# Optimization experiments

Measured on AMD Instinct MI355X. Metric: run time of the kernel, lower is better.

Reference implementation:

```python
import jax, jax.numpy as jnp
import numpy as np

K = 3      # kernel size (fixed by 18 = 2*K*K offset channels)
PAD = 1
EPS = 1e-5 # BatchNorm eps


def setup_inputs() -> dict:
    key = jax.random.key(0)
    ks = jax.random.split(key, 4)
    B, Cin, Cout, H, W = 8, 64, 64, 96, 96
    x = jax.random.normal(ks[0], (B, Cin, H, W), jnp.float32)
    # small offset-conv weights so predicted offsets stay within a few pixels
    w_off = jax.random.normal(ks[1], (2 * K * K, Cin, K, K), jnp.float32) * 0.02
    b_off = jnp.zeros((2 * K * K,), jnp.float32)
    w_def = jax.random.normal(ks[2], (Cout, Cin, K, K), jnp.float32) * (1.0 / np.sqrt(Cin * K * K))
    b_def = jnp.zeros((Cout,), jnp.float32)
    gamma = jnp.ones((Cout,), jnp.float32)
    beta = jnp.zeros((Cout,), jnp.float32)
    return dict(x=x, w_off=w_off, b_off=b_off, w_def=w_def, b_def=b_def, gamma=gamma, beta=beta)


def _deform_sample(x, offset):
    """Bilinear-sample x at deformed kernel tap locations.
    x: (B,C,H,W); offset: (B,2*K*K,H,W) with (dy,dx) pairs per tap, row-major.
    Returns (B,C,K*K,H,W). Out-of-bounds samples are zero (torchvision semantics).
    """
    B, C, H, W = x.shape
    off = offset.reshape(B, K * K, 2, H, W)
    dy, dx = off[:, :, 0], off[:, :, 1]              # (B,9,H,W)
    ky = (jnp.arange(K * K) // K).astype(x.dtype)    # tap row index
    kx = (jnp.arange(K * K) % K).astype(x.dtype)     # tap col index
    base_y = jnp.arange(H, dtype=x.dtype)[:, None] - PAD   # (H,1)
    base_x = jnp.arange(W, dtype=x.dtype)[None, :] - PAD   # (1,W)
    py = dy + ky[None, :, None, None] + base_y[None, None]  # (B,9,H,W)
    px = dx + kx[None, :, None, None] + base_x[None, None]
    y0 = jnp.floor(py)
    x0 = jnp.floor(px)
    wy1 = py - y0
    wx1 = px - x0
    wy0 = 1.0 - wy1
    wx0 = 1.0 - wx1
    xflat = x.reshape(B, C, H * W)
    acc = jnp.zeros((B, C, K * K * H * W), x.dtype)
    corners = [(y0, x0, wy0 * wx0), (y0, x0 + 1.0, wy0 * wx1),
               (y0 + 1.0, x0, wy1 * wx0), (y0 + 1.0, x0 + 1.0, wy1 * wx1)]
    for yc, xc, wc in corners:
        valid = (yc >= 0) & (yc <= H - 1) & (xc >= 0) & (xc <= W - 1)
        iy = jnp.clip(yc, 0, H - 1).astype(jnp.int32)
        ix = jnp.clip(xc, 0, W - 1).astype(jnp.int32)
        idx = (iy * W + ix).reshape(B, 1, K * K * H * W)
        v = jnp.take_along_axis(xflat, idx, axis=2)          # (B,C,9HW) gather
        w = jnp.where(valid, wc, 0.0).reshape(B, 1, K * K * H * W)
        acc = acc + v * w
    return acc.reshape(B, C, K * K, H, W)


def reference(x, w_off, b_off, w_def, b_def, gamma, beta):
    # 1) offset-predicting conv
    offset = jax.lax.conv_general_dilated(
        x, w_off, window_strides=(1, 1), padding=((PAD, PAD), (PAD, PAD)),
        dimension_numbers=("NCHW", "OIHW", "NCHW")) + b_off[None, :, None, None]
    # 2) deformable conv: bilinear gather then per-pixel contraction over (C, taps)
    sampled = _deform_sample(x, offset)                      # (B,C,9,H,W)
    Cout = w_def.shape[0]
    y = jnp.einsum("bckhw,ock->bohw", sampled, w_def.reshape(Cout, -1, K * K))
    y = y + b_def[None, :, None, None]
    # 3) BatchNorm2d (training mode: batch statistics) + ReLU
    mean = y.mean(axis=(0, 2, 3))
    var = y.var(axis=(0, 2, 3))
    y = (y - mean[None, :, None, None]) * jax.lax.rsqrt(var[None, :, None, None] + EPS)
    y = gamma[None, :, None, None] * y + beta[None, :, None, None]
    return jax.nn.relu(y)
```

## Files before the change

### kernel.cpp

```cpp
#include <hip/hip_runtime.h>
#include <hip/hip_bf16.h>
#include <stdint.h>

static constexpr int NBATCH = 8;
static constexpr int Cin  = 64;
static constexpr int Cout = 64;
static constexpr int H = 96, W = 96;
static constexpr int HW   = H * W;
static constexpr int NPIX = NBATCH * HW;
static constexpr int NBLK = NPIX / 64;
static constexpr int BLK_PER_BATCH = HW / 64;
static constexpr float EPS = 1e-5f;

typedef short    bf16x8 __attribute__((ext_vector_type(8)));
typedef float    f32x4  __attribute__((ext_vector_type(4)));
typedef uint32_t u32x4  __attribute__((ext_vector_type(4)));

__device__ inline uint16_t f2bf(float f) {
    __hip_bfloat16 h = __float2bfloat16(f);
    return *reinterpret_cast<uint16_t*>(&h);
}
__device__ inline float bf2f(uint16_t u) {
    union { uint32_t i; float f; } z;
    z.i = ((uint32_t)u) << 16;
    return z.f;
}
__device__ inline float lo_bf(uint32_t w) {
    union { uint32_t i; float f; } z; z.i = w << 16; return z.f;
}
__device__ inline float hi_bf(uint32_t w) {
    union { uint32_t i; float f; } z; z.i = w & 0xffff0000u; return z.f;
}
__device__ inline uint32_t pack_trunc(float lo, float hi) {
    union { float f; uint32_t i; } a, b;
    a.f = lo; b.f = hi;
    return (b.i & 0xffff0000u) | (a.i >> 16);
}
__device__ inline void gld_lds16(const void* g, void* l) {
    __builtin_amdgcn_global_load_lds(
        (const __attribute__((address_space(1))) void*)g,
        (__attribute__((address_space(3))) void*)l, 16, 0, 0);
}

__global__ __launch_bounds__(256) void transpose_pack(
        const float* __restrict__ x,
        const float* __restrict__ w_off,
        const float* __restrict__ w_def,
        uint16_t* __restrict__ xT,
        uint16_t* __restrict__ woffPack,
        uint16_t* __restrict__ wdefPack,
        float* __restrict__ zeropage) {
    int t = blockIdx.x * 256 + threadIdx.x;
    int pix  = t >> 1;
    int half = t & 1;
    int b = pix / HW, rem = pix % HW;
    const float* xb = x + (size_t)(b * Cin) * HW + rem + (size_t)(half * 32) * HW;
    uint16_t* o = xT + (size_t)pix * 64 + half * 32;
#pragma unroll
    for (int cg = 0; cg < 4; ++cg) {
        bf16x8 v;
#pragma unroll
        for (int e = 0; e < 8; ++e) v[e] = (short)f2bf(xb[(cg * 8 + e) * HW]);
        *reinterpret_cast<bf16x8*>(o + cg * 8) = v;
    }
    if (blockIdx.x < 64) {
        int t0 = blockIdx.x * 256 + threadIdx.x;
        if (t0 < 64) zeropage[t0] = 0.f;
        for (int i = t0; i < 72 * 32 * 8; i += 64 * 256) {
            int e = i & 7;
            int n = (i >> 3) & 31;
            int sg = i >> 8;
            int k = sg * 8 + e;
            int tap = k >> 6, c = k & 63;
            woffPack[i] = (n < 18) ? f2bf(w_off[(n * Cin + c) * 9 + tap]) : (uint16_t)0;
        }
        for (int i = t0; i < 72 * 64 * 8; i += 64 * 256) {
            int e = i & 7;
            int n = (i >> 3) & 63;
            int sg = i >> 9;
            int k = sg * 8 + e;
            int tap = k >> 6, c = k & 63;
            wdefPack[i] = f2bf(w_def[(n * Cin + c) * 9 + tap]);
        }
    }
}

#define P3_SETUP(T, W00,W01,W10,W11,I00,I01,I10,I11)                        \
    if ((T) < 8) {                                                          \
        int src_ = lanebase + (T);                                          \
        W00 = __shfl(w00a, src_); W01 = __shfl(w01a, src_);                 \
        W10 = __shfl(w10a, src_); W11 = __shfl(w11a, src_);                 \
        I00 = __shfl(i00a, src_); I01 = __shfl(i01a, src_);                 \
        I10 = __shfl(i10a, src_); I11 = __shfl(i11a, src_);                 \
    } else {                                                                \
        W00 = w00b; W01 = w01b; W10 = w10b; W11 = w11b;                     \
        I00 = i00b; I01 = i01b; I10 = i10b; I11 = i11b;                     \
    }

#define P3_ISSUE(I00,I01,I10,I11,C00,C01,C10,C11)                           \
    C00 = *reinterpret_cast<const u32x4*>(basep + (I00) * 64);              \
    C01 = *reinterpret_cast<const u32x4*>(basep + (I01) * 64);              \
    C10 = *reinterpret_cast<const u32x4*>(basep + (I10) * 64);              \
    C11 = *reinterpret_cast<const u32x4*>(basep + (I11) * 64);

#define P3_CONV(T, W00,W01,W10,W11,C00,C01,C10,C11)                         \
    {                                                                       \
        u32x4 outv_;                                                        \
        _Pragma("unroll")                                                   \
        for (int i = 0; i < 4; ++i) {                                       \
            float slo_ = (W00) * lo_bf((C00)[i]) + (W01) * lo_bf((C01)[i])  \
                       + (W10) * lo_bf((C10)[i]) + (W11) * lo_bf((C11)[i]); \
            float shi_ = (W00) * hi_bf((C00)[i]) + (W01) * hi_bf((C01)[i])  \
                       + (W10) * hi_bf((C10)[i]) + (W11) * hi_bf((C11)[i]); \
            outv_[i] = pack_trunc(slo_, shi_);                              \
        }                                                                   \
        *reinterpret_cast<u32x4*>(&As[(((T) * 64 + pr) * 8 + slot) * 8]) = outv_; \
    }

__global__ __launch_bounds__(512, 4) void fused_deform(
        const uint16_t* __restrict__ xT,
        const uint16_t* __restrict__ woffPack,
        const uint16_t* __restrict__ wdefPack,
        const float* __restrict__ b_off,
        const float* __restrict__ zeropage,
        uint16_t* __restrict__ ybf,
        float* __restrict__ partial) {
    __shared__ __attribute__((aligned(16))) char smem[73728];
    __shared__ float offs[64 * 18];
    __shared__ float s_red[128];
    short* As   = (short*)smem;
    float* osum = (float*)smem;
    float* red  = (float*)smem;

    int tid  = threadIdx.x;
    int lane = tid & 63;
    int wv   = tid >> 6;
    int l15  = lane & 15;
    int lg   = lane >> 4;

    int wgid  = (blockIdx.x & 7) * BLK_PER_BATCH + (blockIdx.x >> 3);
    int gpix0 = wgid * 64;
    int b     = gpix0 / HW;
    int rem0  = gpix0 % HW;
    const uint16_t* xTb = xT + (size_t)b * HW * 64;

    int pr   = (wv << 3) + (lane >> 3);
    int e8   = lane & 7;
    int slot = e8 ^ (pr & 7);
    int remP = rem0 + pr;
    int hP   = remP / W, wP = remP % W;

    {
        const uint16_t* gsrc = xTb + slot * 8;
        char* ldsbase = (char*)As + (size_t)wv * 1024;
#pragma unroll
        for (int tap = 0; tap < 9; ++tap) {
            int yy = hP + tap / 3 - 1;
            int xx = wP + tap % 3 - 1;
            bool ok = (yy >= 0) && (yy < H) && (xx >= 0) && (xx < W);
            const void* g = ok ? (const void*)(gsrc + (yy * W + xx) * 64)
                               : (const void*)zeropage;
            gld_lds16(g, ldsbase + tap * 8192);
        }
    }
    __syncthreads();

    {
        int wj = wv & 1;
        int kq = wv >> 1;
        int sbeg = (kq < 2) ? kq * 5 : 2 + kq * 4;
        int send = (kq < 2) ? sbeg + 5 : sbeg + 4;
        f32x4 oacc[4];
#pragma unroll
        for (int m = 0; m < 4; ++m) oacc[m] = (f32x4){0.f, 0.f, 0.f, 0.f};
        __builtin_amdgcn_s_setprio(1);
        for (int s = sbeg; s < send; ++s) {
            int sg = s * 4 + lg;
            bf16x8 bb = *reinterpret_cast<const bf16x8*>(
                woffPack + (sg * 32 + wj * 16 + l15) * 8);
#pragma unroll
            for (int m = 0; m < 4; ++m) {
                bf16x8 a = *reinterpret_cast<const bf16x8*>(
                    &As[(((sg >> 3) * 64 + m * 16 + l15) * 8 + ((sg & 7) ^ (l15 & 7))) * 8]);
                oacc[m] = __builtin_amdgcn_mfma_f32_16x16x32_bf16(a, bb, oacc[m], 0, 0, 0);
            }
        }
        __builtin_amdgcn_s_setprio(0);
        __syncthreads();
#pragma unroll
        for (int m = 0; m < 4; ++m)
#pragma unroll
            for (int r = 0; r < 4; ++r)
                osum[(kq * 64 + m * 16 + lg * 4 + r) * 34 + wj * 16 + l15] = oacc[m][r];
        __syncthreads();
        for (int i = tid; i < 64 * 18; i += 512) {
            int rr = i / 18, o = i - rr * 18;
            offs[i] = osum[rr * 34 + o] + osum[(64 + rr) * 34 + o]
                    + osum[(128 + rr) * 34 + o] + osum[(192 + rr) * 34 + o] + b_off[o];
        }
        if (tid < 128) s_red[tid] = 0.f;
        __syncthreads();
    }

    {
        float hm1 = (float)(hP - 1), wm1 = (float)(wP - 1);
        float w00a, w01a, w10a, w11a; int i00a, i01a, i10a, i11a;
        {
            int t = e8;
            int ty = (t * 11) >> 5;
            int tx = t - 3 * ty;
            float dy = offs[pr * 18 + 2 * t];
            float dx = offs[pr * 18 + 2 * t + 1];
            float py = dy + (float)ty + hm1;
            float px = dx + (float)tx + wm1;
            float y0f = floorf(py), x0f = floorf(px);
            float wy1 = py - y0f, wx1 = px - x0f;
            float wy0 = 1.f - wy1, wx0 = 1.f - wx1;
            int iy0 = (int)y0f, ix0 = (int)x0f;
            int iy1 = iy0 + 1,  ix1 = ix0 + 1;
            bool vy0 = (iy0 >= 0) && (iy0 < H), vy1 = (iy1 >= 0) && (iy1 < H);
            bool vx0 = (ix0 >= 0) && (ix0 < W), vx1 = (ix1 >= 0) && (ix1 < W);
            w00a = (vy0 && vx0) ? wy0 * wx0 : 0.f;
            w01a = (vy0 && vx1) ? wy0 * wx1 : 0.f;
            w10a = (vy1 && vx0) ? wy1 * wx0 : 0.f;
            w11a = (vy1 && vx1) ? wy1 * wx1 : 0.f;
            int cy0 = min(max(iy0, 0), H - 1), cy1 = min(max(iy1, 0), H - 1);
            int cx0 = min(max(ix0, 0), W - 1), cx1 = min(max(ix1, 0), W - 1);
            i00a = cy0 * W + cx0; i01a = cy0 * W + cx1;
            i10a = cy1 * W + cx0; i11a = cy1 * W + cx1;
        }
        float w00b, w01b, w10b, w11b; int i00b, i01b, i10b, i11b;
        {
            float dy = offs[pr * 18 + 16];
            float dx = offs[pr * 18 + 17];
            float py = dy + 2.f + hm1;
            float px = dx + 2.f + wm1;
            float y0f = floorf(py), x0f = floorf(px);
            float wy1 = py - y0f, wx1 = px - x0f;
            float wy0 = 1.f - wy1, wx0 = 1.f - wx1;
            int iy0 = (int)y0f, ix0 = (int)x0f;
            int iy1 = iy0 + 1,  ix1 = ix0 + 1;
            bool vy0 = (iy0 >= 0) && (iy0 < H), vy1 = (iy1 >= 0) && (iy1 < H);
            bool vx0 = (ix0 >= 0) && (ix0 < W), vx1 = (ix1 >= 0) && (ix1 < W);
            w00b = (vy0 && vx0) ? wy0 * wx0 : 0.f;
            w01b = (vy0 && vx1) ? wy0 * wx1 : 0.f;
            w10b = (vy1 && vx0) ? wy1 * wx0 : 0.f;
            w11b = (vy1 && vx1) ? wy1 * wx1 : 0.f;
            int cy0 = min(max(iy0, 0), H - 1), cy1 = min(max(iy1, 0), H - 1);
            int cx0 = min(max(ix0, 0), W - 1), cx1 = min(max(ix1, 0), W - 1);
            i00b = cy0 * W + cx0; i01b = cy0 * W + cx1;
            i10b = cy1 * W + cx0; i11b = cy1 * W + cx1;
        }

        const uint16_t* basep = xTb + e8 * 8;
        int lanebase = lane & 56;

        float uA0,uA1,uA2,uA3; int jA0,jA1,jA2,jA3; u32x4 cA0,cA1,cA2,cA3;
        float uB0,uB1,uB2,uB3; int jB0,jB1,jB2,jB3; u32x4 cB0,cB1,cB2,cB3;

        P3_SETUP(0, uA0,uA1,uA2,uA3, jA0,jA1,jA2,jA3)
        P3_ISSUE(jA0,jA1,jA2,jA3, cA0,cA1,cA2,cA3)
        P3_SETUP(1, uB0,uB1,uB2,uB3, jB0,jB1,jB2,jB3)
        P3_ISSUE(jB0,jB1,jB2,jB3, cB0,cB1,cB2,cB3)
        P3_CONV(0, uA0,uA1,uA2,uA3, cA0,cA1,cA2,cA3)
        P3_SETUP(2, uA0,uA1,uA2,uA3, jA0,jA1,jA2,jA3)
        P3_ISSUE(jA0,jA1,jA2,jA3, cA0,cA1,cA2,cA3)
        P3_CONV(1, uB0,uB1,uB2,uB3, cB0,cB1,cB2,cB3)
        P3_SETUP(3, uB0,uB1,uB2,uB3, jB0,jB1,jB2,jB3)
        P3_ISSUE(jB0,jB1,jB2,jB3, cB0,cB1,cB2,cB3)
        P3_CONV(2, uA0,uA1,uA2,uA3, cA0,cA1,cA2,cA3)
        P3_SETUP(4, uA0,uA1,uA2,uA3, jA0,jA1,jA2,jA3)
        P3_ISSUE(jA0,jA1,jA2,jA3, cA0,cA1,cA2,cA3)
        P3_CONV(3, uB0,uB1,uB2,uB3, cB0,cB1,cB2,cB3)
        P3_SETUP(5, uB0,uB1,uB2,uB3, jB0,jB1,jB2,jB3)
        P3_ISSUE(jB0,jB1,jB2,jB3, cB0,cB1,cB2,cB3)
        P3_CONV(4, uA0,uA1,uA2,uA3, cA0,cA1,cA2,cA3)
        P3_SETUP(6, uA0,uA1,uA2,uA3, jA0,jA1,jA2,jA3)
        P3_ISSUE(jA0,jA1,jA2,jA3, cA0,cA1,cA2,cA3)
        P3_CONV(5, uB0,uB1,uB2,uB3, cB0,cB1,cB2,cB3)
        P3_SETUP(7, uB0,uB1,uB2,uB3, jB0,jB1,jB2,jB3)
        P3_ISSUE(jB0,jB1,jB2,jB3, cB0,cB1,cB2,cB3)
        P3_CONV(6, uA0,uA1,uA2,uA3, cA0,cA1,cA2,cA3)
        P3_SETUP(8, uA0,uA1,uA2,uA3, jA0,jA1,jA2,jA3)
        P3_ISSUE(jA0,jA1,jA2,jA3, cA0,cA1,cA2,cA3)
        P3_CONV(7, uB0,uB1,uB2,uB3, cB0,cB1,cB2,cB3)
        P3_CONV(8, uA0,uA1,uA2,uA3, cA0,cA1,cA2,cA3)
    }
    __syncthreads();

    {
        int nf = wv & 3;
        int kh = wv >> 2;
        f32x4 acc[4];
#pragma unroll
        for (int m = 0; m < 4; ++m) acc[m] = (f32x4){0.f, 0.f, 0.f, 0.f};
        __builtin_amdgcn_s_setprio(1);
#pragma unroll
        for (int s = 0; s < 9; ++s) {
            int sg = (kh * 9 + s) * 4 + lg;
            bf16x8 bb = *reinterpret_cast<const bf16x8*>(
                wdefPack + (sg * 64 + nf * 16 + l15) * 8);
#pragma unroll
            for (int m = 0; m < 4; ++m) {
                bf16x8 a = *reinterpret_cast<const bf16x8*>(
                    &As[(((sg >> 3) * 64 + m * 16 + l15) * 8 + ((sg & 7) ^ (l15 & 7))) * 8]);
                acc[m] = __builtin_amdgcn_mfma_f32_16x16x32_bf16(a, bb, acc[m], 0, 0, 0);
            }
        }
        __builtin_amdgcn_s_setprio(0);
        __syncthreads();
#pragma unroll
        for (int m = 0; m < 4; ++m)
#pragma unroll
            for (int r = 0; r < 4; ++r)
                red[(kh * 64 + m * 16 + lg * 4 + r) * 66 + nf * 16 + l15] = acc[m][r];
        __syncthreads();

        int c  = lane;
        int rg = wv;
        bf16x8 ov;
        float s = 0.f, q = 0.f;
#pragma unroll
        for (int k2 = 0; k2 < 8; ++k2) {
            int r = rg * 8 + k2;
            float v = red[r * 66 + c] + red[(64 + r) * 66 + c];
            ov[k2] = (short)f2bf(v);
            s += v; q += v * v;
        }
        *reinterpret_cast<bf16x8*>(
            ybf + ((size_t)b * Cout + c) * HW + rem0 + rg * 8) = ov;
        atomicAdd(&s_red[c], s);
        atomicAdd(&s_red[64 + c], q);
    }
    __syncthreads();
    if (tid < 128) partial[(size_t)wgid * 128 + tid] = s_red[tid];
}

__global__ __launch_bounds__(256) void bn_reduce1(const float* __restrict__ partial,
                                                  float* __restrict__ partial2) {
    __shared__ float red[256];
    int ch = threadIdx.x & 127;
    int g  = threadIdx.x >> 7;
    float s = 0.f;
#pragma unroll
    for (int r = 0; r < 8; ++r)
        s += partial[(size_t)(blockIdx.x * 16 + g * 8 + r) * 128 + ch];
    red[threadIdx.x] = s;
    __syncthreads();
    if (g == 0)
        partial2[(size_t)blockIdx.x * 128 + ch] = red[ch] + red[128 + ch];
}

__global__ void bn_stats2(const float* __restrict__ partial2,
                          const float* __restrict__ gamma,
                          const float* __restrict__ beta,
                          float* __restrict__ stats) {
    __shared__ float red[256];
    int ch = threadIdx.x & 127;
    int g  = threadIdx.x >> 7;
    float s = 0.f;
    for (int i = 0; i < 36; ++i)
        s += partial2[(size_t)(g * 36 + i) * 128 + ch];
    red[threadIdx.x] = s;
    __syncthreads();
    if (threadIdx.x < 64) {
        int c = threadIdx.x;
        float sum = red[c] + red[128 + c];
        float sq  = red[64 + c] + red[192 + c];
        float mean = sum / (float)NPIX;
        float var  = sq / (float)NPIX - mean * mean;
        float v    = var + EPS;
        float inv  = rsqrtf(v);
        inv = inv * (1.5f - 0.5f * v * inv * inv);
        float sc = gamma[c] * inv;
        stats[c]      = sc;
        stats[64 + c] = beta[c] - mean * sc;
    }
}

__global__ __launch_bounds__(256) void bn_apply(const uint16_t* __restrict__ ybf,
                                                float* __restrict__ out,
                                                const float* __restrict__ stats) {
    int t = blockIdx.x * blockDim.x + threadIdx.x;
    int e = t * 8;
    int ch = (e / HW) & 63;
    float sc = stats[ch];
    float sh = stats[64 + ch];
    bf16x8 v = *reinterpret_cast<const bf16x8*>(ybf + e);
    f32x4 o0, o1;
#pragma unroll
    for (int i = 0; i < 4; ++i) {
        o0[i] = fmaxf(bf2f((uint16_t)v[i])     * sc + sh, 0.f);
        o1[i] = fmaxf(bf2f((uint16_t)v[4 + i]) * sc + sh, 0.f);
    }
    *reinterpret_cast<f32x4*>(out + e)     = o0;
    *reinterpret_cast<f32x4*>(out + e + 4) = o1;
}

extern "C" void kernel_launch(void* const* d_in, const int* in_sizes, int n_in,
                              void* d_out, int out_size, void* d_ws, size_t ws_size,
                              hipStream_t stream) {
    const float* x     = (const float*)d_in[0];
    const float* w_off = (const float*)d_in[1];
    const float* b_off = (const float*)d_in[2];
    const float* w_def = (const float*)d_in[3];
    const float* gamma = (const float*)d_in[5];
    const float* beta  = (const float*)d_in[6];
    float* out = (float*)d_out;
    char*  ws  = (char*)d_ws;

    uint16_t* xT       = (uint16_t*)ws;
    uint16_t* woffPack = (uint16_t*)(ws + 9437184);
    uint16_t* wdefPack = (uint16_t*)(ws + 9474048);
    float*    partial  = (float*)(ws + 9547776);
    float*    partial2 = (float*)(ws + 10137600);
    float*    stats    = (float*)(ws + 10174464);
    float*    zeropage = (float*)(ws + 10174976);
    uint16_t* ybf      = (uint16_t*)(ws + 10175232);

    transpose_pack<<<NPIX * 2 / 256, 256, 0, stream>>>(x, w_off, w_def, xT,
                                                       woffPack, wdefPack, zeropage);
    fused_deform<<<NBLK, 512, 0, stream>>>(xT, woffPack, wdefPack, b_off,
                                           zeropage, ybf, partial);
    bn_reduce1<<<72, 256, 0, stream>>>(partial, partial2);
    bn_stats2<<<1, 256, 0, stream>>>(partial2, gamma, beta, stats);
    bn_apply<<<(NPIX * Cout / 8) / 256, 256, 0, stream>>>(ybf, out, stats);
}
```

Before: 61.44 us.

## Shrink fused deform tile to 48 pixels with 384-thread blocks and re-split MFMA work

Changes the per-block pixel tile from 64 to 48, using 6 waves (384 threads) instead of 8, and re-partitions both MFMA phases so each wave handles a K-third and two output-column fragments (3x2 accumulators) rather than one. The grid grows to 1536 blocks, which is meant to improve load balance across CUs and reduce LDS per block. The BN reduction launch sizes and workspace offsets are adjusted to match. The trade-off is fewer blocks per CU by launch bounds (3 instead of 4), a three-way K reduction through LDS, and more B-fragment reuse per wave but also more register pressure.

```diff
diff --git a/kernel.cpp b/kernel.cpp
--- a/kernel.cpp
+++ b/kernel.cpp
@@ -8,8 +8,9 @@
 static constexpr int H = 96, W = 96;
 static constexpr int HW   = H * W;
 static constexpr int NPIX = NBATCH * HW;
-static constexpr int NBLK = NPIX / 64;
-static constexpr int BLK_PER_BATCH = HW / 64;
+static constexpr int NTILE = 48;
+static constexpr int NBLK = NPIX / NTILE;
+static constexpr int BLK_PER_BATCH = HW / NTILE;
 static constexpr float EPS = 1e-5f;
 
 typedef short    bf16x8 __attribute__((ext_vector_type(8)));
@@ -114,10 +115,10 @@
                        + (W10) * hi_bf((C10)[i]) + (W11) * hi_bf((C11)[i]); \
             outv_[i] = pack_trunc(slo_, shi_);                              \
         }                                                                   \
-        *reinterpret_cast<u32x4*>(&As[(((T) * 64 + pr) * 8 + slot) * 8]) = outv_; \
-    }
-
-__global__ __launch_bounds__(512, 4) void fused_deform(
+        *reinterpret_cast<u32x4*>(&As[(((T) * NTILE + pr) * 8 + slot) * 8]) = outv_; \
+    }
+
+__global__ __launch_bounds__(384, 3) void fused_deform(
         const uint16_t* __restrict__ xT,
         const uint16_t* __restrict__ woffPack,
         const uint16_t* __restrict__ wdefPack,
@@ -125,8 +126,8 @@
         const float* __restrict__ zeropage,
         uint16_t* __restrict__ ybf,
         float* __restrict__ partial) {
-    __shared__ __attribute__((aligned(16))) char smem[73728];
-    __shared__ float offs[64 * 18];
+    __shared__ __attribute__((aligned(16))) char smem[72 * NTILE * 16];
+    __shared__ float offs[NTILE * 18];
     __shared__ float s_red[128];
     short* As   = (short*)smem;
     float* osum = (float*)smem;
@@ -139,13 +140,12 @@
     int lg   = lane >> 4;
 
     int wgid  = (blockIdx.x & 7) * BLK_PER_BATCH + (blockIdx.x >> 3);
-    int gpix0 = wgid * 64;
-    int b     = gpix0 / HW;
-    int rem0  = gpix0 % HW;
+    int b     = blockIdx.x & 7;
+    int rem0  = (wgid - b * BLK_PER_BATCH) * NTILE;
     const uint16_t* xTb = xT + (size_t)b * HW * 64;
 
-    int pr   = (wv << 3) + (lane >> 3);
-    int e8   = lane & 7;
+    int pr   = tid >> 3;
+    int e8   = tid & 7;
     int slot = e8 ^ (pr & 7);
     int remP = rem0 + pr;
     int hP   = remP / W, wP = remP % W;
@@ -160,43 +160,41 @@
             bool ok = (yy >= 0) && (yy < H) && (xx >= 0) && (xx < W);
             const void* g = ok ? (const void*)(gsrc + (yy * W + xx) * 64)
                                : (const void*)zeropage;
-            gld_lds16(g, ldsbase + tap * 8192);
+            gld_lds16(g, ldsbase + tap * (NTILE * 128));
         }
     }
     __syncthreads();
 
     {
         int wj = wv & 1;
-        int kq = wv >> 1;
-        int sbeg = (kq < 2) ? kq * 5 : 2 + kq * 4;
-        int send = (kq < 2) ? sbeg + 5 : sbeg + 4;
-        f32x4 oacc[4];
-#pragma unroll
-        for (int m = 0; m < 4; ++m) oacc[m] = (f32x4){0.f, 0.f, 0.f, 0.f};
+        int kt = wv >> 1;
+        f32x4 oacc[3];
+#pragma unroll
+        for (int m = 0; m < 3; ++m) oacc[m] = (f32x4){0.f, 0.f, 0.f, 0.f};
         __builtin_amdgcn_s_setprio(1);
-        for (int s = sbeg; s < send; ++s) {
+        for (int s = kt * 6; s < kt * 6 + 6; ++s) {
             int sg = s * 4 + lg;
             bf16x8 bb = *reinterpret_cast<const bf16x8*>(
                 woffPack + (sg * 32 + wj * 16 + l15) * 8);
 #pragma unroll
-            for (int m = 0; m < 4; ++m) {
+            for (int m = 0; m < 3; ++m) {
                 bf16x8 a = *reinterpret_cast<const bf16x8*>(
-                    &As[(((sg >> 3) * 64 + m * 16 + l15) * 8 + ((sg & 7) ^ (l15 & 7))) * 8]);
+                    &As[(((sg >> 3) * NTILE + m * 16 + l15) * 8 + ((sg & 7) ^ (l15 & 7))) * 8]);
                 oacc[m] = __builtin_amdgcn_mfma_f32_16x16x32_bf16(a, bb, oacc[m], 0, 0, 0);
             }
         }
         __builtin_amdgcn_s_setprio(0);
         __syncthreads();
 #pragma unroll
-        for (int m = 0; m < 4; ++m)
+        for (int m = 0; m < 3; ++m)
 #pragma unroll
             for (int r = 0; r < 4; ++r)
-                osum[(kq * 64 + m * 16 + lg * 4 + r) * 34 + wj * 16 + l15] = oacc[m][r];
+                osum[(kt * NTILE + m * 16 + lg * 4 + r) * 34 + wj * 16 + l15] = oacc[m][r];
         __syncthreads();
-        for (int i = tid; i < 64 * 18; i += 512) {
+        for (int i = tid; i < NTILE * 18; i += 384) {
             int rr = i / 18, o = i - rr * 18;
-            offs[i] = osum[rr * 34 + o] + osum[(64 + rr) * 34 + o]
-                    + osum[(128 + rr) * 34 + o] + osum[(192 + rr) * 34 + o] + b_off[o];
+            offs[i] = osum[rr * 34 + o] + osum[(NTILE + rr) * 34 + o]
+                    + osum[(2 * NTILE + rr) * 34 + o] + b_off[o];
         }
         if (tid < 128) s_red[tid] = 0.f;
         __syncthreads();
@@ -289,41 +287,51 @@
     __syncthreads();
 
     {
-        int nf = wv & 3;
-        int kh = wv >> 2;
-        f32x4 acc[4];
-#pragma unroll
-        for (int m = 0; m < 4; ++m) acc[m] = (f32x4){0.f, 0.f, 0.f, 0.f};
+        int npair = wv & 1;
+        int kt = wv >> 1;
+        f32x4 acc[3][2];
+#pragma unroll
+        for (int m = 0; m < 3; ++m)
+#pragma unroll
+            for (int jj = 0; jj < 2; ++jj) acc[m][jj] = (f32x4){0.f, 0.f, 0.f, 0.f};
         __builtin_amdgcn_s_setprio(1);
 #pragma unroll
-        for (int s = 0; s < 9; ++s) {
-            int sg = (kh * 9 + s) * 4 + lg;
-            bf16x8 bb = *reinterpret_cast<const bf16x8*>(
-                wdefPack + (sg * 64 + nf * 16 + l15) * 8);
-#pragma unroll
-            for (int m = 0; m < 4; ++m) {
-                bf16x8 a = *reinterpret_cast<const bf16x8*>(
-                    &As[(((sg >> 3) * 64 + m * 16 + l15) * 8 + ((sg & 7) ^ (l15 & 7))) * 8]);
-                acc[m] = __builtin_amdgcn_mfma_f32_16x16x32_bf16(a, bb, acc[m], 0, 0, 0);
+        for (int s0 = 0; s0 < 6; ++s0) {
+            int sg = (kt * 6 + s0) * 4 + lg;
+#pragma unroll
+            for (int jj = 0; jj < 2; ++jj) {
+                int nf = npair * 2 + jj;
+                bf16x8 bb = *reinterpret_cast<const bf16x8*>(
+                    wdefPack + (sg * 64 + nf * 16 + l15) * 8);
+#pragma unroll
+                for (int m = 0; m < 3; ++m) {
+                    bf16x8 a = *reinterpret_cast<const bf16x8*>(
+                        &As[(((sg >> 3) * NTILE + m * 16 + l15) * 8 + ((sg & 7) ^ (l15 & 7))) * 8]);
+                    acc[m][jj] = __builtin_amdgcn_mfma_f32_16x16x32_bf16(a, bb, acc[m][jj], 0, 0, 0);
+                }
             }
         }
         __builtin_amdgcn_s_setprio(0);
         __syncthreads();
 #pragma unroll
-        for (int m = 0; m < 4; ++m)
-#pragma unroll
-            for (int r = 0; r < 4; ++r)
-                red[(kh * 64 + m * 16 + lg * 4 + r) * 66 + nf * 16 + l15] = acc[m][r];
+        for (int m = 0; m < 3; ++m)
+#pragma unroll
+            for (int jj = 0; jj < 2; ++jj)
+#pragma unroll
+                for (int r = 0; r < 4; ++r)
+                    red[(kt * NTILE + m * 16 + lg * 4 + r) * 66
+                        + (npair * 2 + jj) * 16 + l15] = acc[m][jj][r];
         __syncthreads();
 
-        int c  = lane;
-        int rg = wv;
+        int c  = tid & 63;
+        int rg = tid >> 6;
         bf16x8 ov;
         float s = 0.f, q = 0.f;
 #pragma unroll
         for (int k2 = 0; k2 < 8; ++k2) {
             int r = rg * 8 + k2;
-            float v = red[r * 66 + c] + red[(64 + r) * 66 + c];
+            float v = red[r * 66 + c] + red[(NTILE + r) * 66 + c]
+                    + red[(2 * NTILE + r) * 66 + c];
             ov[k2] = (short)f2bf(v);
             s += v; q += v * v;
         }
@@ -359,8 +367,8 @@
     int ch = threadIdx.x & 127;
     int g  = threadIdx.x >> 7;
     float s = 0.f;
-    for (int i = 0; i < 36; ++i)
-        s += partial2[(size_t)(g * 36 + i) * 128 + ch];
+    for (int i = 0; i < 48; ++i)
+        s += partial2[(size_t)(g * 48 + i) * 128 + ch];
     red[threadIdx.x] = s;
     __syncthreads();
     if (threadIdx.x < 64) {
@@ -413,16 +421,16 @@
     uint16_t* woffPack = (uint16_t*)(ws + 9437184);
     uint16_t* wdefPack = (uint16_t*)(ws + 9474048);
     float*    partial  = (float*)(ws + 9547776);
-    float*    partial2 = (float*)(ws + 10137600);
-    float*    stats    = (float*)(ws + 10174464);
-    float*    zeropage = (float*)(ws + 10174976);
-    uint16_t* ybf      = (uint16_t*)(ws + 10175232);
+    float*    partial2 = (float*)(ws + 10334208);
+    float*    stats    = (float*)(ws + 10383360);
+    float*    zeropage = (float*)(ws + 10383872);
+    uint16_t* ybf      = (uint16_t*)(ws + 10384128);
 
     transpose_pack<<<NPIX * 2 / 256, 256, 0, stream>>>(x, w_off, w_def, xT,
                                                        woffPack, wdefPack, zeropage);
-    fused_deform<<<NBLK, 512, 0, stream>>>(xT, woffPack, wdefPack, b_off,
+    fused_deform<<<NBLK, 384, 0, stream>>>(xT, woffPack, wdefPack, b_off,
                                            zeropage, ybf, partial);
-    bn_reduce1<<<72, 256, 0, stream>>>(partial, partial2);
+    bn_reduce1<<<96, 256, 0, stream>>>(partial, partial2);
     bn_stats2<<<1, 256, 0, stream>>>(partial2, gamma, beta, stats);
     bn_apply<<<(NPIX * Cout / 8) / 256, 256, 0, stream>>>(ybf, out, stats);
 }
```

After: 74.36 us. +21.0%, slower.

## Repartition MFMA work across waves to drop split-K LDS reductions

Applied to the files above, without the earlier changes.

Both GEMM phases (offset conv and deformable conv) now split work across waves by M/N tiles, each wave running the full K loop, instead of splitting K and reducing partial sums through shared memory. This removes the LDS staging of partial accumulators and several __syncthreads barriers. Results go straight from registers into offs and to global memory with bf16x4 stores, and the BN partial sums are reduced with wave shuffles. In exchange each wave runs a longer serial MFMA chain with less independent accumulation, and the global stores are narrower.

```diff
diff --git a/kernel.cpp b/kernel.cpp
--- a/kernel.cpp
+++ b/kernel.cpp
@@ -13,6 +13,7 @@
 static constexpr float EPS = 1e-5f;
 
 typedef short    bf16x8 __attribute__((ext_vector_type(8)));
+typedef short    bf16x4 __attribute__((ext_vector_type(4)));
 typedef float    f32x4  __attribute__((ext_vector_type(4)));
 typedef uint32_t u32x4  __attribute__((ext_vector_type(4)));
 
@@ -128,9 +129,7 @@
     __shared__ __attribute__((aligned(16))) char smem[73728];
     __shared__ float offs[64 * 18];
     __shared__ float s_red[128];
-    short* As   = (short*)smem;
-    float* osum = (float*)smem;
-    float* red  = (float*)smem;
+    short* As = (short*)smem;
 
     int tid  = threadIdx.x;
     int lane = tid & 63;
@@ -149,6 +148,8 @@
     int slot = e8 ^ (pr & 7);
     int remP = rem0 + pr;
     int hP   = remP / W, wP = remP % W;
+
+    if (tid < 128) s_red[tid] = 0.f;
 
     {
         const uint16_t* gsrc = xTb + slot * 8;
@@ -167,40 +168,28 @@
 
     {
         int wj = wv & 1;
-        int kq = wv >> 1;
-        int sbeg = (kq < 2) ? kq * 5 : 2 + kq * 4;
-        int send = (kq < 2) ? sbeg + 5 : sbeg + 4;
-        f32x4 oacc[4];
-#pragma unroll
-        for (int m = 0; m < 4; ++m) oacc[m] = (f32x4){0.f, 0.f, 0.f, 0.f};
+        int m  = wv >> 1;
+        f32x4 oacc = (f32x4){0.f, 0.f, 0.f, 0.f};
         __builtin_amdgcn_s_setprio(1);
-        for (int s = sbeg; s < send; ++s) {
+#pragma unroll 6
+        for (int s = 0; s < 18; ++s) {
             int sg = s * 4 + lg;
             bf16x8 bb = *reinterpret_cast<const bf16x8*>(
                 woffPack + (sg * 32 + wj * 16 + l15) * 8);
-#pragma unroll
-            for (int m = 0; m < 4; ++m) {
-                bf16x8 a = *reinterpret_cast<const bf16x8*>(
-                    &As[(((sg >> 3) * 64 + m * 16 + l15) * 8 + ((sg & 7) ^ (l15 & 7))) * 8]);
-                oacc[m] = __builtin_amdgcn_mfma_f32_16x16x32_bf16(a, bb, oacc[m], 0, 0, 0);
-            }
+            bf16x8 a = *reinterpret_cast<const bf16x8*>(
+                &As[(((sg >> 3) * 64 + m * 16 + l15) * 8 + ((sg & 7) ^ (l15 & 7))) * 8]);
+            oacc = __builtin_amdgcn_mfma_f32_16x16x32_bf16(a, bb, oacc, 0, 0, 0);
         }
         __builtin_amdgcn_s_setprio(0);
-        __syncthreads();
-#pragma unroll
-        for (int m = 0; m < 4; ++m)
+        int o = wj * 16 + l15;
+        if (o < 18) {
+            float bo = b_off[o];
 #pragma unroll
             for (int r = 0; r < 4; ++r)
-                osum[(kq * 64 + m * 16 + lg * 4 + r) * 34 + wj * 16 + l15] = oacc[m][r];
-        __syncthreads();
-        for (int i = tid; i < 64 * 18; i += 512) {
-            int rr = i / 18, o = i - rr * 18;
-            offs[i] = osum[rr * 34 + o] + osum[(64 + rr) * 34 + o]
-                    + osum[(128 + rr) * 34 + o] + osum[(192 + rr) * 34 + o] + b_off[o];
-        }
-        if (tid < 128) s_red[tid] = 0.f;
-        __syncthreads();
-    }
+                offs[(m * 16 + lg * 4 + r) * 18 + o] = oacc[r] + bo;
+        }
+    }
+    __syncthreads();
 
     {
         float hm1 = (float)(hP - 1), wm1 = (float)(wP - 1);
@@ -290,47 +279,53 @@
 
     {
         int nf = wv & 3;
-        int kh = wv >> 2;
-        f32x4 acc[4];
-#pragma unroll
-        for (int m = 0; m < 4; ++m) acc[m] = (f32x4){0.f, 0.f, 0.f, 0.f};
+        int mp = wv >> 2;
+        f32x4 acc0 = (f32x4){0.f, 0.f, 0.f, 0.f};
+        f32x4 acc1 = (f32x4){0.f, 0.f, 0.f, 0.f};
         __builtin_amdgcn_s_setprio(1);
-#pragma unroll
-        for (int s = 0; s < 9; ++s) {
-            int sg = (kh * 9 + s) * 4 + lg;
+#pragma unroll 6
+        for (int s = 0; s < 18; ++s) {
+            int sg = s * 4 + lg;
             bf16x8 bb = *reinterpret_cast<const bf16x8*>(
                 wdefPack + (sg * 64 + nf * 16 + l15) * 8);
-#pragma unroll
-            for (int m = 0; m < 4; ++m) {
-                bf16x8 a = *reinterpret_cast<const bf16x8*>(
-                    &As[(((sg >> 3) * 64 + m * 16 + l15) * 8 + ((sg & 7) ^ (l15 & 7))) * 8]);
-                acc[m] = __builtin_amdgcn_mfma_f32_16x16x32_bf16(a, bb, acc[m], 0, 0, 0);
+            bf16x8 a0 = *reinterpret_cast<const bf16x8*>(
+                &As[(((sg >> 3) * 64 + (mp * 2) * 16 + l15) * 8 + ((sg & 7) ^ (l15 & 7))) * 8]);
+            bf16x8 a1 = *reinterpret_cast<const bf16x8*>(
+                &As[(((sg >> 3) * 64 + (mp * 2 + 1) * 16 + l15) * 8 + ((sg & 7) ^ (l15 & 7))) * 8]);
+            acc0 = __builtin_amdgcn_mfma_f32_16x16x32_bf16(a0, bb, acc0, 0, 0, 0);
+            acc1 = __builtin_amdgcn_mfma_f32_16x16x32_bf16(a1, bb, acc1, 0, 0, 0);
+        }
+        __builtin_amdgcn_s_setprio(0);
+
+        int cout = nf * 16 + l15;
+        uint16_t* yrow = ybf + ((size_t)b * Cout + cout) * HW + rem0;
+        float s = 0.f, q = 0.f;
+        {
+            bf16x4 ov;
+#pragma unroll
+            for (int r = 0; r < 4; ++r) {
+                float v = acc0[r];
+                ov[r] = (short)f2bf(v);
+                s += v; q += v * v;
             }
-        }
-        __builtin_amdgcn_s_setprio(0);
-        __syncthreads();
-#pragma unroll
-        for (int m = 0; m < 4; ++m)
-#pragma unroll
-            for (int r = 0; r < 4; ++r)
-                red[(kh * 64 + m * 16 + lg * 4 + r) * 66 + nf * 16 + l15] = acc[m][r];
-        __syncthreads();
-
-        int c  = lane;
-        int rg = wv;
-        bf16x8 ov;
-        float s = 0.f, q = 0.f;
-#pragma unroll
-        for (int k2 = 0; k2 < 8; ++k2) {
-            int r = rg * 8 + k2;
-            float v = red[r * 66 + c] + red[(64 + r) * 66 + c];
-            ov[k2] = (short)f2bf(v);
-            s += v; q += v * v;
-        }
-        *reinterpret_cast<bf16x8*>(
-            ybf + ((size_t)b * Cout + c) * HW + rem0 + rg * 8) = ov;
-        atomicAdd(&s_red[c], s);
-        atomicAdd(&s_red[64 + c], q);
+            *reinterpret_cast<bf16x4*>(yrow + (mp * 2) * 16 + lg * 4) = ov;
+        }
+        {
+            bf16x4 ov;
+#pragma unroll
+            for (int r = 0; r < 4; ++r) {
+                float v = acc1[r];
+                ov[r] = (short)f2bf(v);
+                s += v; q += v * v;
+            }
+            *reinterpret_cast<bf16x4*>(yrow + (mp * 2 + 1) * 16 + lg * 4) = ov;
+        }
+        s += __shfl_xor(s, 16); s += __shfl_xor(s, 32);
+        q += __shfl_xor(q, 16); q += __shfl_xor(q, 32);
+        if (lg == 0) {
+            atomicAdd(&s_red[cout], s);
+            atomicAdd(&s_red[64 + cout], q);
+        }
     }
     __syncthreads();
     if (tid < 128) partial[(size_t)wgid * 128 + tid] = s_red[tid];
```

New measurement: 57.25 us. 6.8% less time.
